# Kernel tuning notes

Hardware: AMD Instinct MI355X
Metric: run time of the kernel (lower is better)

Reference implementation:

```python
import jax, jax.numpy as jnp
import numpy as np

N_NODES = 100000
N_EDGES = 600000
D_IN = 128
D_HID = 128


def gcn_conv(x, W, b, src, dst, n_nodes):
    # PyG GCNConv: add self-loops, symmetric deg^-1/2 normalization,
    # linear transform, scatter-add aggregation, bias.
    xw = x @ W  # [N, H]
    self_loop = jnp.arange(n_nodes, dtype=src.dtype)
    s = jnp.concatenate([src, self_loop])  # sources j
    d = jnp.concatenate([dst, self_loop])  # targets i
    deg = jax.ops.segment_sum(jnp.ones_like(d, dtype=xw.dtype), d,
                              num_segments=n_nodes)
    dinv = jnp.where(deg > 0, jax.lax.rsqrt(deg), 0.0)
    norm = dinv[s] * dinv[d]  # [E+N]
    msg = xw[s] * norm[:, None]  # gather + scale
    out = jax.ops.segment_sum(msg, d, num_segments=n_nodes)
    return out + b


def setup_inputs() -> dict:
    key = jax.random.key(0)
    ks = jax.random.split(key, 4)
    x = jax.random.normal(ks[0], (N_NODES, D_IN), dtype=jnp.float32)
    edge_index = jax.random.randint(ks[1], (2, N_EDGES), 0, N_NODES,
                                    dtype=jnp.int32)
    W1 = jax.random.normal(ks[2], (D_IN, D_HID), dtype=jnp.float32) / np.sqrt(D_IN)
    b1 = jnp.zeros((D_HID,), dtype=jnp.float32)
    W2 = jax.random.normal(ks[3], (D_HID, D_HID), dtype=jnp.float32) / np.sqrt(D_HID)
    b2 = jnp.zeros((D_HID,), dtype=jnp.float32)
    return {"x": x, "edge_index": edge_index, "W1": W1, "b1": b1,
            "W2": W2, "b2": b2}


def reference(x, edge_index, W1, b1, W2, b2):
    src, dst = edge_index[0], edge_index[1]
    n = x.shape[0]
    z = gcn_conv(x, W1, b1, src, dst, n)
    z = jax.nn.relu(z)
    z = gcn_conv(z, W2, b2, src, dst, n)
    # decode: per-edge dot product of endpoint embeddings
    return jnp.sum(z[src] * z[dst], axis=1)  # [E]
```

## Files before the change

kernel.cpp:

```cpp
#include <hip/hip_runtime.h>


typedef __attribute__((ext_vector_type(8))) short short8;
typedef __attribute__((ext_vector_type(4))) float f32x4;

__device__ __forceinline__ unsigned bf16_rne(float x) {
  unsigned u = __builtin_bit_cast(unsigned, x);
  return (u + 0x7FFFu + ((u >> 16) & 1u)) >> 16;
}
__device__ __forceinline__ float bf2f(unsigned short u) {
  return __builtin_bit_cast(float, ((unsigned)u) << 16);
}

__global__ __launch_bounds__(256) void deg_kernel(const int* __restrict__ dst,
                                                  int* __restrict__ deg, int E) {
  int base = blockIdx.x * 1024 + threadIdx.x;
#pragma unroll
  for (int i = 0; i < 4; ++i) {
    int e = base + i * 256;
    if (e < E) atomicAdd(&deg[dst[e]], 1);
  }
}

__global__ __launch_bounds__(512) void scan1_kernel(const int* __restrict__ in,
                                                    int* __restrict__ tmp,
                                                    int* __restrict__ bsums, int n) {
  __shared__ int sm[2][512];
  int t = threadIdx.x;
  int gid = blockIdx.x * 512 + t;
  int v = (gid < n) ? in[gid] : 0;
  int pp = 0;
  sm[0][t] = v;
  __syncthreads();
  for (int off = 1; off < 512; off <<= 1) {
    int nv = sm[pp][t];
    if (t >= off) nv += sm[pp][t - off];
    sm[pp ^ 1][t] = nv;
    pp ^= 1;
    __syncthreads();
  }
  int inc = sm[pp][t];
  if (gid < n) tmp[gid] = inc;
  if (t == 511) bsums[blockIdx.x] = inc;
}

__global__ __launch_bounds__(256) void scan2_kernel(int* bsums, int nb) {
  __shared__ int sm[2][256];
  int t = threadIdx.x;
  int v = (t < nb) ? bsums[t] : 0;
  int pp = 0;
  sm[0][t] = v;
  __syncthreads();
  for (int off = 1; off < 256; off <<= 1) {
    int nv = sm[pp][t];
    if (t >= off) nv += sm[pp][t - off];
    sm[pp ^ 1][t] = nv;
    pp ^= 1;
    __syncthreads();
  }
  int inc = sm[pp][t];
  if (t < nb) bsums[t] = inc - v;
}

__global__ __launch_bounds__(256) void scan3_kernel(const int* __restrict__ tmp,
                                                    const int* __restrict__ bsums,
                                                    const int* __restrict__ deg,
                                                    int* __restrict__ rowptr,
                                                    float* __restrict__ dinv, int n) {
  int gid = blockIdx.x * 256 + threadIdx.x;
  if (gid < n) {
    rowptr[gid + 1] = tmp[gid] + bsums[gid >> 9];
    dinv[gid] = rsqrtf((float)(deg[gid] + 1));
  }
  if (gid == 0) rowptr[0] = 0;
}

__global__ __launch_bounds__(256) void scatter_kernel(const int* __restrict__ src,
                                                      const int* __restrict__ dst,
                                                      const int* __restrict__ rowptr,
                                                      int* __restrict__ cnt,
                                                      int2* __restrict__ csr, int E) {
  int base = blockIdx.x * 1024 + threadIdx.x;
#pragma unroll
  for (int i = 0; i < 4; ++i) {
    int e = base + i * 256;
    if (e < E) {
      int d = dst[e];
      int pos = rowptr[d] + atomicAdd(&cnt[d], 1);
      csr[pos] = make_int2(src[e], e);
    }
  }
}

__global__ __launch_bounds__(256) void wpack_kernel(const float* __restrict__ W,
                                                    short* __restrict__ Wp) {
  int t = blockIdx.x * 256 + threadIdx.x;
  if (t >= 2048) return;
  int lane = t & 63;
  int kf = (t >> 6) & 3;
  int ct = t >> 8;
  int col = ct * 16 + (lane & 15);
  int k0 = kf * 32 + (lane >> 4) * 8;
  short* dh = Wp + ((((0 * 8 + ct) * 4 + kf) * 64) + lane) * 8;
  short* dl = Wp + ((((1 * 8 + ct) * 4 + kf) * 64) + lane) * 8;
  for (int j = 0; j < 8; ++j) {
    float w = W[(k0 + j) * 128 + col];
    unsigned h = bf16_rne(w);
    float hf = __builtin_bit_cast(float, h << 16);
    unsigned lo = bf16_rne(w - hf);
    dh[j] = (short)h;
    dl[j] = (short)lo;
  }
}

template <bool FP32A>
__global__ __launch_bounds__(256) void gemm_kernel(const void* __restrict__ Av,
                                                   const short* __restrict__ Wp,
                                                   const float* __restrict__ dinv,
                                                   unsigned short* __restrict__ out,
                                                   int M) {
  const int wave = threadIdx.x >> 6;
  const int lane = threadIdx.x & 63;
  const int quad = lane >> 4;
  const int l15 = lane & 15;

  short8 Bh[2][4], Bl[2][4];
  const short8* Wp8 = (const short8*)Wp;
#pragma unroll
  for (int c = 0; c < 2; ++c) {
    int ct = wave * 2 + c;
#pragma unroll
    for (int f = 0; f < 4; ++f) {
      Bh[c][f] = Wp8[((0 * 8 + ct) * 4 + f) * 64 + lane];
      Bl[c][f] = Wp8[((1 * 8 + ct) * 4 + f) * 64 + lane];
    }
  }

  int rb0 = blockIdx.x * 64;
  const int colbase = wave * 32 + l15;
#pragma unroll 1
  for (int s = 0; s < 4; ++s) {
    int rb = rb0 + s * 16;
    if (rb >= M) break;
    int arow = rb + l15;
    bool rok = arow < M;
    short8 af[4];
#pragma unroll
    for (int f = 0; f < 4; ++f) {
      if (rok) {
        if constexpr (FP32A) {
          const float4* A4 = (const float4*)Av + (size_t)arow * 32;
          float4 a0 = A4[f * 8 + quad * 2];
          float4 a1 = A4[f * 8 + quad * 2 + 1];
          float av[8] = {a0.x, a0.y, a0.z, a0.w, a1.x, a1.y, a1.z, a1.w};
#pragma unroll
          for (int j = 0; j < 8; ++j) af[f][j] = (short)bf16_rne(av[j]);
        } else {
          af[f] = *(const short8*)((const unsigned short*)Av +
                                   (size_t)arow * 128 + f * 32 + quad * 8);
        }
      } else {
        short8 z = {0, 0, 0, 0, 0, 0, 0, 0};
        af[f] = z;
      }
    }
    f32x4 acc0 = {0.f, 0.f, 0.f, 0.f};
    f32x4 acc1 = {0.f, 0.f, 0.f, 0.f};
#pragma unroll
    for (int f = 0; f < 4; ++f) {
      acc0 = __builtin_amdgcn_mfma_f32_16x16x32_bf16(af[f], Bh[0][f], acc0, 0, 0, 0);
      acc1 = __builtin_amdgcn_mfma_f32_16x16x32_bf16(af[f], Bh[1][f], acc1, 0, 0, 0);
      acc0 = __builtin_amdgcn_mfma_f32_16x16x32_bf16(af[f], Bl[0][f], acc0, 0, 0, 0);
      acc1 = __builtin_amdgcn_mfma_f32_16x16x32_bf16(af[f], Bl[1][f], acc1, 0, 0, 0);
    }
#pragma unroll
    for (int i = 0; i < 4; ++i) {
      int r = rb + quad * 4 + i;
      if (r < M) {
        float d = dinv[r];
        out[(size_t)r * 128 + colbase] = (unsigned short)bf16_rne(acc0[i] * d);
        out[(size_t)r * 128 + colbase + 16] = (unsigned short)bf16_rne(acc1[i] * d);
      }
    }
  }
}

__global__ __launch_bounds__(256) void agg_kernel(const unsigned short* __restrict__ xw,
                                                  const float* __restrict__ dinv,
                                                  const int* __restrict__ rowptr,
                                                  const int2* __restrict__ csr,
                                                  const float* __restrict__ bias,
                                                  unsigned short* __restrict__ out,
                                                  int relu, int N) {
  int node = blockIdx.x * 16 + (threadIdx.x >> 4);
  int l = threadIdx.x & 15;
  if (node >= N) return;
  const short8* xw8 = (const short8*)xw;
  short8 sv = xw8[(size_t)node * 16 + l];
  float acc[8];
#pragma unroll
  for (int j = 0; j < 8; ++j) acc[j] = bf2f((unsigned short)sv[j]);
  int s = rowptr[node], e = rowptr[node + 1];
  int k = s;
  for (; k + 4 <= e; k += 4) {
    int j0 = csr[k].x, j1 = csr[k + 1].x, j2 = csr[k + 2].x, j3 = csr[k + 3].x;
    short8 v0 = xw8[(size_t)j0 * 16 + l];
    short8 v1 = xw8[(size_t)j1 * 16 + l];
    short8 v2 = xw8[(size_t)j2 * 16 + l];
    short8 v3 = xw8[(size_t)j3 * 16 + l];
#pragma unroll
    for (int j = 0; j < 8; ++j) {
      acc[j] += (bf2f((unsigned short)v0[j]) + bf2f((unsigned short)v1[j])) +
                (bf2f((unsigned short)v2[j]) + bf2f((unsigned short)v3[j]));
    }
  }
  for (; k < e; ++k) {
    short8 v = xw8[(size_t)csr[k].x * 16 + l];
#pragma unroll
    for (int j = 0; j < 8; ++j) acc[j] += bf2f((unsigned short)v[j]);
  }
  float di = dinv[node];
  const float4* b4 = (const float4*)bias;
  float4 bb0 = b4[l * 2], bb1 = b4[l * 2 + 1];
  float bv[8] = {bb0.x, bb0.y, bb0.z, bb0.w, bb1.x, bb1.y, bb1.z, bb1.w};
  short8 o;
#pragma unroll
  for (int j = 0; j < 8; ++j) {
    float v = fmaf(di, acc[j], bv[j]);
    if (relu) v = fmaxf(v, 0.f);
    o[j] = (short)bf16_rne(v);
  }
  ((short8*)out)[(size_t)node * 16 + l] = o;
}

__global__ __launch_bounds__(256) void decode_kernel(const unsigned short* __restrict__ z,
                                                     const int* __restrict__ rowptr,
                                                     const int2* __restrict__ csr,
                                                     float* __restrict__ out, int N) {
  int node = blockIdx.x * 16 + (threadIdx.x >> 4);
  int l = threadIdx.x & 15;
  if (node >= N) return;
  const short8* z8 = (const short8*)z;
  short8 zv = z8[(size_t)node * 16 + l];
  float zd[8];
#pragma unroll
  for (int j = 0; j < 8; ++j) zd[j] = bf2f((unsigned short)zv[j]);
  int s = rowptr[node], e = rowptr[node + 1];
  int k = s;
  for (; k + 4 <= e; k += 4) {
    int2 c0 = csr[k], c1 = csr[k + 1], c2 = csr[k + 2], c3 = csr[k + 3];
    short8 v0 = z8[(size_t)c0.x * 16 + l];
    short8 v1 = z8[(size_t)c1.x * 16 + l];
    short8 v2 = z8[(size_t)c2.x * 16 + l];
    short8 v3 = z8[(size_t)c3.x * 16 + l];
    float p0 = 0.f, p1 = 0.f, p2 = 0.f, p3 = 0.f;
#pragma unroll
    for (int j = 0; j < 8; ++j) {
      p0 = fmaf(zd[j], bf2f((unsigned short)v0[j]), p0);
      p1 = fmaf(zd[j], bf2f((unsigned short)v1[j]), p1);
      p2 = fmaf(zd[j], bf2f((unsigned short)v2[j]), p2);
      p3 = fmaf(zd[j], bf2f((unsigned short)v3[j]), p3);
    }
#pragma unroll
    for (int off = 8; off > 0; off >>= 1) {
      p0 += __shfl_xor(p0, off);
      p1 += __shfl_xor(p1, off);
      p2 += __shfl_xor(p2, off);
      p3 += __shfl_xor(p3, off);
    }
    if (l == 0) {
      out[c0.y] = p0;
      out[c1.y] = p1;
      out[c2.y] = p2;
      out[c3.y] = p3;
    }
  }
  for (; k < e; ++k) {
    int2 c = csr[k];
    short8 v = z8[(size_t)c.x * 16 + l];
    float p = 0.f;
#pragma unroll
    for (int j = 0; j < 8; ++j) p = fmaf(zd[j], bf2f((unsigned short)v[j]), p);
#pragma unroll
    for (int off = 8; off > 0; off >>= 1) p += __shfl_xor(p, off);
    if (l == 0) out[c.y] = p;
  }
}

extern "C" void kernel_launch(void* const* d_in, const int* in_sizes, int n_in,
                              void* d_out, int out_size, void* d_ws, size_t ws_size,
                              hipStream_t stream) {
  const float* x  = (const float*)d_in[0];
  const int*   ei = (const int*)d_in[1];
  const float* W1 = (const float*)d_in[2];
  const float* b1 = (const float*)d_in[3];
  const float* W2 = (const float*)d_in[4];
  const float* b2 = (const float*)d_in[5];

  const int N = in_sizes[0] / 128;
  const int E = in_sizes[1] / 2;
  const int* src = ei;
  const int* dst = ei + E;

  char* ws = (char*)d_ws;
  size_t off = 0;
  auto alloc = [&](size_t bytes) -> void* {
    void* p = ws + off;
    off += (bytes + 255) & ~(size_t)255;
    return p;
  };
  unsigned short* bufA = (unsigned short*)alloc((size_t)N * 128 * 2);
  unsigned short* bufB = (unsigned short*)alloc((size_t)N * 128 * 2);
  float* dinv    = (float*)alloc((size_t)N * 4);
  int*   rowptr  = (int*)alloc((size_t)(N + 1) * 4);
  int2*  csr     = (int2*)alloc((size_t)E * 8);
  short* Wp1     = (short*)alloc((size_t)2 * 8 * 4 * 64 * 8 * 2);
  short* Wp2     = (short*)alloc((size_t)2 * 8 * 4 * 64 * 8 * 2);
  int*   tmp     = (int*)alloc((size_t)N * 4);
  int*   deg     = (int*)alloc((size_t)N * 4);
  int*   cnt     = (int*)alloc((size_t)N * 4);
  int*   bsums   = (int*)alloc(1024);
  size_t zbytes = ((char*)bsums + 1024) - (char*)deg;
  hipMemsetAsync(deg, 0, zbytes, stream);

  const int E4B = (E + 1023) / 1024;
  const int NB = (N + 255) / 256;
  const int SB = (N + 511) / 512;

  wpack_kernel<<<8, 256, 0, stream>>>(W1, Wp1);
  wpack_kernel<<<8, 256, 0, stream>>>(W2, Wp2);

  deg_kernel<<<E4B, 256, 0, stream>>>(dst, deg, E);
  scan1_kernel<<<SB, 512, 0, stream>>>(deg, tmp, bsums, N);
  scan2_kernel<<<1, 256, 0, stream>>>(bsums, SB);
  scan3_kernel<<<NB, 256, 0, stream>>>(tmp, bsums, deg, rowptr, dinv, N);
  scatter_kernel<<<E4B, 256, 0, stream>>>(src, dst, rowptr, cnt, csr, E);

  const int GB = (N + 63) / 64;
  const int AB = (N + 15) / 16;
  const int DB = (N + 15) / 16;

  gemm_kernel<true><<<GB, 256, 0, stream>>>(x, Wp1, dinv, bufA, N);
  agg_kernel<<<AB, 256, 0, stream>>>(bufA, dinv, rowptr, csr, b1, bufB, 1, N);
  gemm_kernel<false><<<GB, 256, 0, stream>>>(bufB, Wp2, dinv, bufA, N);
  agg_kernel<<<AB, 256, 0, stream>>>(bufA, dinv, rowptr, csr, b2, bufB, 0, N);
  decode_kernel<<<DB, 256, 0, stream>>>(bufB, rowptr, csr, (float*)d_out, N);
}
```

Measured before the change: 323.3 us.

## Stage packed weights in LDS and process two row tiles per GEMM step

The GEMM kernel now copies the packed hi/lo bf16 weight fragments (64KB) into shared memory once per block instead of holding them in registers. Each iteration handles 32 rows as two 16-row tiles that share the B fragments, and each block now covers 256 rows instead of 64, so there are fewer blocks and fewer weight reloads. The trade-off is 64KB of LDS per block, which limits occupancy, plus LDS reads of B inside the k loop.

```diff
diff --git a/kernel.cpp b/kernel.cpp
--- a/kernel.cpp
+++ b/kernel.cpp
@@ -114,72 +114,98 @@
 }
 
 template <bool FP32A>
-__global__ __launch_bounds__(256) void gemm_kernel(const void* __restrict__ Av,
-                                                   const short* __restrict__ Wp,
-                                                   const float* __restrict__ dinv,
-                                                   unsigned short* __restrict__ out,
-                                                   int M) {
-  const int wave = threadIdx.x >> 6;
-  const int lane = threadIdx.x & 63;
+__global__ __launch_bounds__(256, 2) void gemm_kernel(const void* __restrict__ Av,
+                                                      const short* __restrict__ Wp,
+                                                      const float* __restrict__ dinv,
+                                                      unsigned short* __restrict__ out,
+                                                      int M) {
+  __shared__ short8 lds_w[4096];
+
+  const int tid = threadIdx.x;
+  {
+    const short8* Wg = (const short8*)Wp;
+#pragma unroll
+    for (int i = 0; i < 16; ++i) lds_w[i * 256 + tid] = Wg[i * 256 + tid];
+  }
+  __syncthreads();
+
+  const int wave = tid >> 6;
+  const int lane = tid & 63;
   const int quad = lane >> 4;
   const int l15 = lane & 15;
-
-  short8 Bh[2][4], Bl[2][4];
-  const short8* Wp8 = (const short8*)Wp;
-#pragma unroll
-  for (int c = 0; c < 2; ++c) {
-    int ct = wave * 2 + c;
-#pragma unroll
-    for (int f = 0; f < 4; ++f) {
-      Bh[c][f] = Wp8[((0 * 8 + ct) * 4 + f) * 64 + lane];
-      Bl[c][f] = Wp8[((1 * 8 + ct) * 4 + f) * 64 + lane];
-    }
-  }
-
-  int rb0 = blockIdx.x * 64;
   const int colbase = wave * 32 + l15;
+  const short8* WL = (const short8*)lds_w;
+
+  const int rb0 = blockIdx.x * 256;
+  const short8 s8z = {0, 0, 0, 0, 0, 0, 0, 0};
+
 #pragma unroll 1
-  for (int s = 0; s < 4; ++s) {
-    int rb = rb0 + s * 16;
+  for (int ss = 0; ss < 8; ++ss) {
+    const int rb = rb0 + ss * 32;
     if (rb >= M) break;
-    int arow = rb + l15;
-    bool rok = arow < M;
-    short8 af[4];
-#pragma unroll
-    for (int f = 0; f < 4; ++f) {
-      if (rok) {
-        if constexpr (FP32A) {
-          const float4* A4 = (const float4*)Av + (size_t)arow * 32;
-          float4 a0 = A4[f * 8 + quad * 2];
-          float4 a1 = A4[f * 8 + quad * 2 + 1];
-          float av[8] = {a0.x, a0.y, a0.z, a0.w, a1.x, a1.y, a1.z, a1.w};
-#pragma unroll
-          for (int j = 0; j < 8; ++j) af[f][j] = (short)bf16_rne(av[j]);
-        } else {
-          af[f] = *(const short8*)((const unsigned short*)Av +
-                                   (size_t)arow * 128 + f * 32 + quad * 8);
+
+    short8 af[2][4];
+#pragma unroll
+    for (int mt = 0; mt < 2; ++mt) {
+      const int arow = rb + mt * 16 + l15;
+      const bool rok = arow < M;
+      if constexpr (FP32A) {
+        const float4* A4 = (const float4*)Av + (size_t)arow * 32;
+#pragma unroll
+        for (int f = 0; f < 4; ++f) {
+          if (rok) {
+            float4 a0 = A4[f * 8 + quad * 2];
+            float4 a1 = A4[f * 8 + quad * 2 + 1];
+            float av[8] = {a0.x, a0.y, a0.z, a0.w, a1.x, a1.y, a1.z, a1.w};
+#pragma unroll
+            for (int j = 0; j < 8; ++j) af[mt][f][j] = (short)bf16_rne(av[j]);
+          } else {
+            af[mt][f] = s8z;
+          }
         }
       } else {
-        short8 z = {0, 0, 0, 0, 0, 0, 0, 0};
-        af[f] = z;
+        const unsigned short* A2 = (const unsigned short*)Av + (size_t)arow * 128;
+#pragma unroll
+        for (int f = 0; f < 4; ++f)
+          af[mt][f] = rok ? *(const short8*)(A2 + f * 32 + quad * 8) : s8z;
       }
     }
-    f32x4 acc0 = {0.f, 0.f, 0.f, 0.f};
-    f32x4 acc1 = {0.f, 0.f, 0.f, 0.f};
-#pragma unroll
-    for (int f = 0; f < 4; ++f) {
-      acc0 = __builtin_amdgcn_mfma_f32_16x16x32_bf16(af[f], Bh[0][f], acc0, 0, 0, 0);
-      acc1 = __builtin_amdgcn_mfma_f32_16x16x32_bf16(af[f], Bh[1][f], acc1, 0, 0, 0);
-      acc0 = __builtin_amdgcn_mfma_f32_16x16x32_bf16(af[f], Bl[0][f], acc0, 0, 0, 0);
-      acc1 = __builtin_amdgcn_mfma_f32_16x16x32_bf16(af[f], Bl[1][f], acc1, 0, 0, 0);
-    }
-#pragma unroll
-    for (int i = 0; i < 4; ++i) {
-      int r = rb + quad * 4 + i;
-      if (r < M) {
-        float d = dinv[r];
-        out[(size_t)r * 128 + colbase] = (unsigned short)bf16_rne(acc0[i] * d);
-        out[(size_t)r * 128 + colbase + 16] = (unsigned short)bf16_rne(acc1[i] * d);
+
+    f32x4 acc[2][2];
+#pragma unroll
+    for (int mt = 0; mt < 2; ++mt)
+#pragma unroll
+      for (int c = 0; c < 2; ++c) acc[mt][c] = (f32x4){0.f, 0.f, 0.f, 0.f};
+
+#pragma unroll
+    for (int kf = 0; kf < 4; ++kf) {
+#pragma unroll
+      for (int c = 0; c < 2; ++c) {
+        const int ct = wave * 2 + c;
+        short8 bh = WL[((0 * 8 + ct) * 4 + kf) * 64 + lane];
+        short8 bl = WL[((1 * 8 + ct) * 4 + kf) * 64 + lane];
+#pragma unroll
+        for (int mt = 0; mt < 2; ++mt) {
+          acc[mt][c] =
+              __builtin_amdgcn_mfma_f32_16x16x32_bf16(af[mt][kf], bh, acc[mt][c], 0, 0, 0);
+          acc[mt][c] =
+              __builtin_amdgcn_mfma_f32_16x16x32_bf16(af[mt][kf], bl, acc[mt][c], 0, 0, 0);
+        }
+      }
+    }
+
+#pragma unroll
+    for (int mt = 0; mt < 2; ++mt) {
+      const int rbm = rb + mt * 16;
+#pragma unroll
+      for (int i = 0; i < 4; ++i) {
+        const int r = rbm + quad * 4 + i;
+        if (r < M) {
+          const float d = dinv[r];
+          out[(size_t)r * 128 + colbase] = (unsigned short)bf16_rne(acc[mt][0][i] * d);
+          out[(size_t)r * 128 + colbase + 16] =
+              (unsigned short)bf16_rne(acc[mt][1][i] * d);
+        }
       }
     }
   }
@@ -336,7 +362,7 @@
   scan3_kernel<<<NB, 256, 0, stream>>>(tmp, bsums, deg, rowptr, dinv, N);
   scatter_kernel<<<E4B, 256, 0, stream>>>(src, dst, rowptr, cnt, csr, E);
 
-  const int GB = (N + 63) / 64;
+  const int GB = (N + 255) / 256;
   const int AB = (N + 15) / 16;
   const int DB = (N + 15) / 16;
 
```

Result: slower. 354.0 us (+9.5%).
